# Kernel tuning notes

Measured on AMD Instinct MI355X. Metric: run time of the kernel, lower is better.

## Reference

```python
import jax, jax.numpy as jnp
import numpy as np

B, H, W, EMB = 8, 128, 128, 6
NF = 256  # number_of_filters


def setup_inputs() -> dict:
    key = jax.random.key(0)
    ks = jax.random.split(key, 12)
    s = 0.02  # init_func-style small normal init
    image = jax.random.normal(ks[0], (B, 1, H, W), jnp.float32)
    mask_embedding = jax.random.normal(ks[1], (B, EMB, H, W), jnp.float32)
    # conv stack: 134->256 (s2), 256->512 (s2), 512->1024 (s2), 1024->1024 (s2), avgpool8, 1024->128 (1x1)
    w0 = jax.random.normal(ks[2], (NF, W + EMB, 4, 4), jnp.float32) * s
    b0 = jnp.zeros((NF,), jnp.float32)
    w1 = jax.random.normal(ks[3], (2 * NF, NF, 4, 4), jnp.float32) * s
    b1 = jnp.zeros((2 * NF,), jnp.float32)
    w2 = jax.random.normal(ks[4], (4 * NF, 2 * NF, 4, 4), jnp.float32) * s
    b2 = jnp.zeros((4 * NF,), jnp.float32)
    w3 = jax.random.normal(ks[5], (4 * NF, 4 * NF, 4, 4), jnp.float32) * s
    b3 = jnp.zeros((4 * NF,), jnp.float32)
    w4 = jax.random.normal(ks[6], (W, 4 * NF, 1, 1), jnp.float32) * s
    b4 = jnp.zeros((W,), jnp.float32)
    return dict(image=image, mask_embedding=mask_embedding,
                w0=w0, b0=b0, w1=w1, b1=b1, w2=w2, b2=b2, w3=w3, b3=b3, w4=w4, b4=b4)


def _spectral_map(image, mask_embedding):
    # Original: kspace = fft2(image); for each column i zero out all other k-space
    # columns, ifft2 (unnormalized torch.ifft => 1/(H*W)), take real part.
    # Since only column i is nonzero, ifft2 separates:
    #   sep[b,i,h,w] = Re( (1/W) * ifft_H(kspace[:, :, i])[h] * exp(2j*pi*w*i/W) )
    Bv, _, Hv, Wv = image.shape
    kspace = jnp.fft.fft2(image[:, 0])                    # (B, H, W) complex64
    col = jnp.fft.ifft(kspace, axis=1) / Wv               # (B, H, W_i); ifft over height gives 1/H
    idx = jnp.arange(Wv)
    twiddle = jnp.exp((2j * jnp.pi / Wv) * jnp.outer(idx, idx).astype(jnp.float32))  # (W_spatial, W_i) complex64
    sep = jnp.real(jnp.einsum('bhi,wi->bihw', col, twiddle))  # (B, W, H, W) float32
    return jnp.concatenate([sep, mask_embedding], axis=1)     # (B, W+EMB, H, W)


def _conv(x, w, b, stride):
    y = jax.lax.conv_general_dilated(x, w, (stride, stride), [(1, 1), (1, 1)],
                                     dimension_numbers=('NCHW', 'OIHW', 'NCHW'))
    return y + b[None, :, None, None]


def _inorm(x):  # InstanceNorm2d, affine=False, eps=1e-5
    m = jnp.mean(x, (2, 3), keepdims=True)
    v = jnp.var(x, (2, 3), keepdims=True)
    return (x - m) * jax.lax.rsqrt(v + 1e-5)


def _lrelu(x):
    return jax.nn.leaky_relu(x, 0.2)


def reference(image, mask_embedding, w0, b0, w1, b1, w2, b2, w3, b3, w4, b4):
    x = _spectral_map(image, mask_embedding)       # (B, 134, 128, 128)
    x = _lrelu(_conv(x, w0, b0, 2))                # (B, 256, 64, 64)
    x = _lrelu(_inorm(_conv(x, w1, b1, 2)))        # (B, 512, 32, 32)
    x = _lrelu(_inorm(_conv(x, w2, b2, 2)))        # (B, 1024, 16, 16)
    x = _lrelu(_inorm(_conv(x, w3, b3, 2)))        # (B, 1024, 8, 8)
    pooled = jnp.mean(x, (2, 3))                   # AvgPool(k=8) -> (B, 1024)
    out = jnp.einsum('bc,oc->bo', pooled, w4[:, :, 0, 0]) + b4  # 1x1 conv + squeeze -> (B, 128)
    return out
```

## Files before the change

kernel.cpp:

```cpp
#include <hip/hip_runtime.h>
#include <hip/hip_bf16.h>
#include <cstdint>
#include <cstddef>

typedef __attribute__((ext_vector_type(8))) short bf16x8;
typedef __attribute__((ext_vector_type(4))) float f32x4;

#define PI2F 6.283185307179586f

__device__ __forceinline__ float bf2f(unsigned short u) {
  union { float f; uint32_t i; } x; x.i = ((uint32_t)u) << 16; return x.f;
}
__device__ __forceinline__ unsigned short f2bf(float f) {
  union { float f; uint32_t i; } x; x.f = f;
  uint32_t r = x.i + 0x7FFF + ((x.i >> 16) & 1);
  return (unsigned short)(r >> 16);
}

__device__ __forceinline__ void glds16(const void* g, void* l) {
  __builtin_amdgcn_global_load_lds(
      (const __attribute__((address_space(1))) unsigned int*)g,
      (__attribute__((address_space(3))) unsigned int*)l, 16, 0, 0);
}

__global__ void zinit_kernel(unsigned short* __restrict__ zp, unsigned short* __restrict__ pad) {
  int t = threadIdx.x;
  zp[t] = 0;
  pad[t] = 0;
}

__global__ void dft_kernel(const float* __restrict__ img, float2* __restrict__ col,
                           float2* __restrict__ tw) {
  __shared__ float row[128];
  __shared__ float2 twl[128];
  const int bh = blockIdx.x;
  const int i = threadIdx.x;
  row[i] = img[bh * 128 + i];
  float s, c;
  sincosf(PI2F * (float)i / 128.0f, &s, &c);
  twl[i] = make_float2(c, s);
  __syncthreads();
  if (bh == 0) tw[i] = twl[i];
  float sr = 0.f, si = 0.f;
  for (int w = 0; w < 128; ++w) {
    float v = row[w];
    float2 t = twl[(i * w) & 127];
    sr += v * t.x;
    si -= v * t.y;
  }
  col[bh * 128 + i] = make_float2(sr * (1.0f / 128.0f), si * (1.0f / 128.0f));
}

__global__ __launch_bounds__(256)
void sep_cl2_kernel(const float2* __restrict__ col, const float2* __restrict__ tw,
                    const float* __restrict__ maskE, unsigned short* __restrict__ x0) {
  __shared__ float2 cl[128];
  __shared__ float2 twl[128];
  const int bh = blockIdx.x;
  const int b = bh >> 7, h = bh & 127;
  const int tid = threadIdx.x;
  if (tid < 128) {
    cl[tid] = col[(b * 128 + h) * 128 + tid];
    twl[tid] = tw[tid];
  }
  __syncthreads();
  const int p = tid >> 1;
  const int c0 = (tid & 1) * 64;
  unsigned short* dst = x0 + ((size_t)bh * 128 + p) * 144;
#pragma unroll
  for (int j = 0; j < 16; ++j) {
    ushort4 o;
#pragma unroll
    for (int q = 0; q < 4; ++q) {
      int c = c0 + 4 * j + q;
      float2 cv = cl[c];
      float2 t = twl[(p * c) & 127];
      float v = cv.x * t.x - cv.y * t.y;
      ((unsigned short*)&o)[q] = f2bf(v);
    }
    *reinterpret_cast<ushort4*>(dst + c0 + 4 * j) = o;
  }
  if (tid < 128) {
    const int w = tid;
    float v[6];
#pragma unroll
    for (int cm = 0; cm < 6; ++cm)
      v[cm] = maskE[(((size_t)(b * 6 + cm) * 128) + h) * 128 + w];
    unsigned short* d2 = x0 + ((size_t)bh * 128 + w) * 144 + 128;
    ushort4 m0, m1, mz;
    m0.x = f2bf(v[0]); m0.y = f2bf(v[1]); m0.z = f2bf(v[2]); m0.w = f2bf(v[3]);
    m1.x = f2bf(v[4]); m1.y = f2bf(v[5]); m1.z = 0; m1.w = 0;
    mz.x = 0; mz.y = 0; mz.z = 0; mz.w = 0;
    reinterpret_cast<ushort4*>(d2)[0] = m0;
    reinterpret_cast<ushort4*>(d2)[1] = m1;
    reinterpret_cast<ushort4*>(d2)[2] = mz;
    reinterpret_cast<ushort4*>(d2)[3] = mz;
  }
}

template<int CIN, int CINP>
__global__ __launch_bounds__(256)
void cvtperm_kernel(const float* __restrict__ src, unsigned short* __restrict__ dst) {
  __shared__ unsigned short tile[16][68];
  const int m = blockIdx.y;
  const int ci0 = blockIdx.x * 64;
  const int tid = threadIdx.x;
  {
    const int ci = ci0 + (tid >> 2);
    const int t0 = (tid & 3) * 4;
    float4 v = make_float4(0.f, 0.f, 0.f, 0.f);
    if (ci < CIN) v = *reinterpret_cast<const float4*>(&src[((size_t)m * CIN + ci) * 16 + t0]);
    const int cr = tid >> 2;
    tile[t0 + 0][cr] = f2bf(v.x);
    tile[t0 + 1][cr] = f2bf(v.y);
    tile[t0 + 2][cr] = f2bf(v.z);
    tile[t0 + 3][cr] = f2bf(v.w);
  }
  __syncthreads();
  {
    const int t = tid >> 4;
    const int co = (tid & 15) * 4;
    const int ci = ci0 + co;
    if (ci < CINP) {
      ushort4 o;
      o.x = tile[t][co]; o.y = tile[t][co + 1]; o.z = tile[t][co + 2]; o.w = tile[t][co + 3];
      *reinterpret_cast<ushort4*>(&dst[(size_t)m * (16 * CINP) + (size_t)t * CINP + ci]) = o;
    }
  }
}

template<int CINP, int CSTOR, int COUT, int HI, int WI, int HO, int WO, int NSPLIT, bool FUSED>
__global__ __launch_bounds__(128, 2)
void conv_cl6_kernel(const unsigned short* __restrict__ X,
                     const unsigned short* __restrict__ Wt,
                     const unsigned short* __restrict__ zp,
                     const float* __restrict__ bias,
                     unsigned short* __restrict__ Y,
                     float* __restrict__ P) {
  constexpr int KTOT = 16 * CINP;
  constexpr int CPT = CINP / 32;
  constexpr int HOWO = HO * WO;
  constexpr int LHW = __builtin_ctz(HOWO);
  constexpr int LWO = __builtin_ctz(WO);
  constexpr int TPS = 16 / NSPLIT;
  constexpr size_t PSTRIDE = (size_t)8 * HOWO * COUT;
  constexpr int NIT = TPS * CPT;

  __shared__ __align__(16) unsigned short As[3][4096];
  __shared__ __align__(16) unsigned short Bs[3][2048];

  const int tid = threadIdx.x;
  const int lane = tid & 63;
  const int wv = tid >> 6;
  const int n0 = blockIdx.x * 64;
  const int m0 = blockIdx.y * 128;
  const int split = blockIdx.z;
  const int r = lane & 15, g = lane >> 4;
  const int slot = (((g + ((r >> 1) & 3)) & 3)) * 8;

  const int sr = tid >> 2;
  const int chk = tid & 3;
  const int kofs = (((chk - ((sr >> 1) & 3)) & 3)) * 8;

  int bb0, bho0, bwo0, bb1, bho1, bwo1;
  {
    int rn0 = n0 + sr, rn1 = n0 + sr + 32;
    bb0 = rn0 >> LHW; bb1 = rn1 >> LHW;
    int re0 = rn0 & (HOWO - 1), re1 = rn1 & (HOWO - 1);
    bho0 = re0 >> LWO; bho1 = re1 >> LWO;
    bwo0 = re0 & (WO - 1); bwo1 = re1 & (WO - 1);
  }

  const int tap0 = split * TPS;
  int tapI = tap0, ccI = 0;
  size_t boff0, boff1; bool bok0, bok1;
  auto tap_geom = [&](int t) {
    int kh = t >> 2, kw = t & 3;
    {
      int h = 2 * bho0 - 1 + kh, w = 2 * bwo0 - 1 + kw;
      bool hv = (unsigned)h < (unsigned)HI, wvv = (unsigned)w < (unsigned)WI;
      bok0 = hv && wvv;
      boff0 = (((size_t)bb0 * HI + (hv ? h : 0)) * WI + (wvv ? w : 0)) * (size_t)CSTOR;
    }
    {
      int h = 2 * bho1 - 1 + kh, w = 2 * bwo1 - 1 + kw;
      bool hv = (unsigned)h < (unsigned)HI, wvv = (unsigned)w < (unsigned)WI;
      bok1 = hv && wvv;
      boff1 = (((size_t)bb1 * HI + (hv ? h : 0)) * WI + (wvv ? w : 0)) * (size_t)CSTOR;
    }
  };
  tap_geom(tapI);

  auto issue = [&](int buf) {
    const int kk = tapI * CINP + ccI * 32 + kofs;
    const unsigned short* wb = Wt + (size_t)(m0 + sr) * KTOT + kk;
    glds16(wb,                       &As[buf][(wv * 16) * 32]);
    glds16(wb + (size_t)32 * KTOT,   &As[buf][(32 + wv * 16) * 32]);
    glds16(wb + (size_t)64 * KTOT,   &As[buf][(64 + wv * 16) * 32]);
    glds16(wb + (size_t)96 * KTOT,   &As[buf][(96 + wv * 16) * 32]);
    const int ci = ccI * 32 + kofs;
    glds16(bok0 ? (X + boff0 + ci) : zp, &Bs[buf][(wv * 16) * 32]);
    glds16(bok1 ? (X + boff1 + ci) : zp, &Bs[buf][(32 + wv * 16) * 32]);
  };
  auto advance = [&]() {
    ccI++;
    if (ccI == CPT) { ccI = 0; tapI++; if (tapI < tap0 + TPS) tap_geom(tapI); }
  };

  f32x4 acc[4][4] = {};

  issue(0); advance();
  issue(1); advance();

  int buf = 0, nbuf = 2;
  for (int it = 0; it < NIT; ++it) {
    if (it + 1 < NIT) asm volatile("s_waitcnt vmcnt(6)" ::: "memory");
    else              asm volatile("s_waitcnt vmcnt(0)" ::: "memory");
    __builtin_amdgcn_s_barrier();
    __builtin_amdgcn_sched_barrier(0);
    if (it + 2 < NIT) { issue(nbuf); advance(); }
    bf16x8 af[4], bf[4];
#pragma unroll
    for (int mi = 0; mi < 4; ++mi)
      af[mi] = *reinterpret_cast<const bf16x8*>(&As[buf][(wv * 64 + mi * 16 + r) * 32 + slot]);
#pragma unroll
    for (int ni = 0; ni < 4; ++ni)
      bf[ni] = *reinterpret_cast<const bf16x8*>(&Bs[buf][(ni * 16 + r) * 32 + slot]);
    __builtin_amdgcn_s_setprio(1);
#pragma unroll
    for (int mi = 0; mi < 4; ++mi)
#pragma unroll
      for (int ni = 0; ni < 4; ++ni)
        acc[mi][ni] = __builtin_amdgcn_mfma_f32_16x16x32_bf16(af[mi], bf[ni], acc[mi][ni], 0, 0, 0);
    __builtin_amdgcn_s_setprio(0);
    buf = buf == 2 ? 0 : buf + 1;
    nbuf = nbuf == 2 ? 0 : nbuf + 1;
  }

#pragma unroll
  for (int ni = 0; ni < 4; ++ni) {
    int n = n0 + ni * 16 + r;
    int b = n >> LHW;
    int rem = n & (HOWO - 1);
    size_t obase = ((size_t)b * HOWO + rem) * COUT;
#pragma unroll
    for (int mi = 0; mi < 4; ++mi) {
      int mb = m0 + wv * 64 + mi * 16 + g * 4;
      f32x4 a = acc[mi][ni];
      if constexpr (FUSED) {
        float v0 = a[0] + bias[mb + 0]; v0 = v0 > 0.f ? v0 : 0.2f * v0;
        float v1 = a[1] + bias[mb + 1]; v1 = v1 > 0.f ? v1 : 0.2f * v1;
        float v2 = a[2] + bias[mb + 2]; v2 = v2 > 0.f ? v2 : 0.2f * v2;
        float v3 = a[3] + bias[mb + 3]; v3 = v3 > 0.f ? v3 : 0.2f * v3;
        ushort4 o;
        o.x = f2bf(v0); o.y = f2bf(v1); o.z = f2bf(v2); o.w = f2bf(v3);
        *reinterpret_cast<ushort4*>(&Y[obase + mb]) = o;
      } else {
        *reinterpret_cast<float4*>(&P[split * PSTRIDE + obase + mb]) =
            make_float4(a[0], a[1], a[2], a[3]);
      }
    }
  }
}

template<int HOWO, int COUT, int NSPLIT>
__global__ __launch_bounds__(256)
void inorm_cl3_kernel(const float* __restrict__ P, unsigned short* __restrict__ Y) {
  constexpr int PER = HOWO / 32;
  constexpr size_t PSTRIDE = (size_t)8 * HOWO * COUT;
  const int b = blockIdx.y;
  const int cl = threadIdx.x & 7;
  const int c = blockIdx.x * 8 + cl;
  const int hw0 = threadIdx.x >> 3;
  const float* base = P + ((size_t)b * HOWO) * COUT + c;
  float v[PER];
  float s1 = 0.f, s2 = 0.f;
#pragma unroll
  for (int j = 0; j < PER; ++j) {
    int hw = hw0 + j * 32;
    float x = 0.f;
#pragma unroll
    for (int s = 0; s < NSPLIT; ++s) x += base[s * PSTRIDE + (size_t)hw * COUT];
    v[j] = x; s1 += x; s2 += x * x;
  }
  __shared__ float r1[32][9], r2[32][9];
  __shared__ float ms[8], rs[8];
  r1[hw0][cl] = s1; r2[hw0][cl] = s2;
  __syncthreads();
  if (threadIdx.x < 8) {
    float a1 = 0.f, a2 = 0.f;
#pragma unroll
    for (int i = 0; i < 32; ++i) { a1 += r1[i][threadIdx.x]; a2 += r2[i][threadIdx.x]; }
    float mean = a1 * (1.0f / HOWO);
    float var = a2 * (1.0f / HOWO) - mean * mean;
    ms[threadIdx.x] = mean;
    rs[threadIdx.x] = rsqrtf(var + 1e-5f);
  }
  __syncthreads();
  const float mean = ms[cl], rstd = rs[cl];
  unsigned short* yb = Y + ((size_t)b * HOWO) * COUT + c;
#pragma unroll
  for (int j = 0; j < PER; ++j) {
    int hw = hw0 + j * 32;
    float t = (v[j] - mean) * rstd;
    t = t > 0.f ? t : 0.2f * t;
    yb[(size_t)hw * COUT] = f2bf(t);
  }
}

__global__ __launch_bounds__(256)
void pool_cl_kernel(const unsigned short* __restrict__ X, float* __restrict__ pooled) {
  const int b = blockIdx.x;
  const int c4 = threadIdx.x * 4;
  float4 acc = make_float4(0.f, 0.f, 0.f, 0.f);
  for (int hw = 0; hw < 64; ++hw) {
    ushort4 v = *reinterpret_cast<const ushort4*>(&X[((size_t)b * 64 + hw) * 1024 + c4]);
    acc.x += bf2f(v.x); acc.y += bf2f(v.y); acc.z += bf2f(v.z); acc.w += bf2f(v.w);
  }
  acc.x *= (1.0f / 64.0f); acc.y *= (1.0f / 64.0f);
  acc.z *= (1.0f / 64.0f); acc.w *= (1.0f / 64.0f);
  *reinterpret_cast<float4*>(&pooled[b * 1024 + c4]) = acc;
}

__global__ __launch_bounds__(64)
void fc_kernel(const float* __restrict__ pooled, const float* __restrict__ w4,
               const float* __restrict__ b4, float* __restrict__ out) {
  const int bo = blockIdx.x;
  const int b = bo >> 7, o = bo & 127;
  const int lane = threadIdx.x;
  float s = 0.f;
#pragma unroll
  for (int j = 0; j < 16; ++j) {
    int c = lane + j * 64;
    s += pooled[b * 1024 + c] * w4[o * 1024 + c];
  }
#pragma unroll
  for (int off = 32; off > 0; off >>= 1) s += __shfl_xor(s, off);
  if (lane == 0) out[bo] = s + b4[o];
}

extern "C" void kernel_launch(void* const* d_in, const int* in_sizes, int n_in,
                              void* d_out, int out_size, void* d_ws, size_t ws_size,
                              hipStream_t stream) {
  (void)in_sizes; (void)n_in; (void)out_size; (void)ws_size;
  const float* image = (const float*)d_in[0];
  const float* maskE = (const float*)d_in[1];
  const float* w0 = (const float*)d_in[2];
  const float* b0 = (const float*)d_in[3];
  const float* w1 = (const float*)d_in[4];
  const float* w2 = (const float*)d_in[6];
  const float* w3 = (const float*)d_in[8];
  const float* w4 = (const float*)d_in[10];
  const float* b4 = (const float*)d_in[11];
  float* out = (float*)d_out;

  char* ws = (char*)d_ws;
  size_t off = 0;
  auto alloc = [&](size_t bytes) -> void* {
    void* p = ws + off;
    off = (off + bytes + 255) & ~(size_t)255;
    return p;
  };

  const size_t X0BYTES = (size_t)8 * 128 * 128 * 144 * 2;
  unsigned short* wbuf = (unsigned short*)alloc((size_t)1024 * 16384 * 2);
  char* bufA = (char*)alloc(X0BYTES + 256);
  char* bufB = (char*)alloc((size_t)8 * 4096 * 256 * 2);
  float2* col = (float2*)alloc((size_t)131072 * sizeof(float2));
  float2* tw = (float2*)alloc(128 * sizeof(float2));
  float* pooled = (float*)alloc(8192 * 4);
  unsigned short* zp = (unsigned short*)alloc(256);

  unsigned short* x0 = (unsigned short*)bufA;
  unsigned short* x0pad = (unsigned short*)(bufA + X0BYTES);
  float* part = (float*)bufA;
  unsigned short* a0 = (unsigned short*)bufB;
  unsigned short* a1 = (unsigned short*)bufB;
  unsigned short* a2 = (unsigned short*)bufB;
  unsigned short* a3 = (unsigned short*)bufB;

  zinit_kernel<<<1, 128, 0, stream>>>(zp, x0pad);

  dft_kernel<<<1024, 128, 0, stream>>>(image, col, tw);
  sep_cl2_kernel<<<1024, 256, 0, stream>>>(col, tw, maskE, x0);

  cvtperm_kernel<134, 160><<<dim3(3, 256), 256, 0, stream>>>(w0, wbuf);
  conv_cl6_kernel<160, 144, 256, 128, 128, 64, 64, 1, true>
      <<<dim3(512, 2, 1), 128, 0, stream>>>(x0, wbuf, zp, b0, a0, nullptr);

  cvtperm_kernel<256, 256><<<dim3(4, 512), 256, 0, stream>>>(w1, wbuf);
  conv_cl6_kernel<256, 256, 512, 64, 64, 32, 32, 2, false>
      <<<dim3(128, 4, 2), 128, 0, stream>>>(a0, wbuf, zp, nullptr, nullptr, part);
  inorm_cl3_kernel<1024, 512, 2><<<dim3(64, 8), 256, 0, stream>>>(part, a1);

  cvtperm_kernel<512, 512><<<dim3(8, 1024), 256, 0, stream>>>(w2, wbuf);
  conv_cl6_kernel<512, 512, 1024, 32, 32, 16, 16, 4, false>
      <<<dim3(32, 8, 4), 128, 0, stream>>>(a1, wbuf, zp, nullptr, nullptr, part);
  inorm_cl3_kernel<256, 1024, 4><<<dim3(128, 8), 256, 0, stream>>>(part, a2);

  cvtperm_kernel<1024, 1024><<<dim3(16, 1024), 256, 0, stream>>>(w3, wbuf);
  conv_cl6_kernel<1024, 1024, 1024, 16, 16, 8, 8, 16, false>
      <<<dim3(8, 8, 16), 128, 0, stream>>>(a2, wbuf, zp, nullptr, nullptr, part);
  inorm_cl3_kernel<64, 1024, 16><<<dim3(128, 8), 256, 0, stream>>>(part, a3);

  pool_cl_kernel<<<8, 256, 0, stream>>>(a3, pooled);
  fc_kernel<<<1024, 64, 0, stream>>>(pooled, w4, b4, out);
}
```

Measured before the change: 368.7 us.

## Use 4 waves per conv block with 2x2 warp tiling and double buffering

The implicit-GEMM conv kernel moves from 2 waves (each computing 64x64) to 4 waves arranged 2x2 (each computing 64x32). Each thread now issues fewer async global-to-LDS loads, and the accumulator count per thread is halved. The pipeline drops from triple buffering with explicit vmcnt waits to double buffering with a plain __syncthreads, which shrinks LDS use and allows higher occupancy. The cost is less prefetch depth, so global load latency is hidden less well, and the setprio hints are removed.

```diff
diff --git a/kernel.cpp b/kernel.cpp
--- a/kernel.cpp
+++ b/kernel.cpp
@@ -130,8 +130,8 @@
 }
 
 template<int CINP, int CSTOR, int COUT, int HI, int WI, int HO, int WO, int NSPLIT, bool FUSED>
-__global__ __launch_bounds__(128, 2)
-void conv_cl6_kernel(const unsigned short* __restrict__ X,
+__global__ __launch_bounds__(256, 4)
+void conv_cl7_kernel(const unsigned short* __restrict__ X,
                      const unsigned short* __restrict__ Wt,
                      const unsigned short* __restrict__ zp,
                      const float* __restrict__ bias,
@@ -146,12 +146,13 @@
   constexpr size_t PSTRIDE = (size_t)8 * HOWO * COUT;
   constexpr int NIT = TPS * CPT;
 
-  __shared__ __align__(16) unsigned short As[3][4096];
-  __shared__ __align__(16) unsigned short Bs[3][2048];
+  __shared__ __align__(16) unsigned short As[2][4096];
+  __shared__ __align__(16) unsigned short Bs[2][2048];
 
   const int tid = threadIdx.x;
   const int lane = tid & 63;
   const int wv = tid >> 6;
+  const int wm = wv >> 1, wn = wv & 1;
   const int n0 = blockIdx.x * 64;
   const int m0 = blockIdx.y * 128;
   const int split = blockIdx.z;
@@ -162,90 +163,70 @@
   const int chk = tid & 3;
   const int kofs = (((chk - ((sr >> 1) & 3)) & 3)) * 8;
 
-  int bb0, bho0, bwo0, bb1, bho1, bwo1;
+  int bb, bho, bwo;
   {
-    int rn0 = n0 + sr, rn1 = n0 + sr + 32;
-    bb0 = rn0 >> LHW; bb1 = rn1 >> LHW;
-    int re0 = rn0 & (HOWO - 1), re1 = rn1 & (HOWO - 1);
-    bho0 = re0 >> LWO; bho1 = re1 >> LWO;
-    bwo0 = re0 & (WO - 1); bwo1 = re1 & (WO - 1);
+    int rn = n0 + sr;
+    bb = rn >> LHW;
+    int re = rn & (HOWO - 1);
+    bho = re >> LWO;
+    bwo = re & (WO - 1);
   }
 
   const int tap0 = split * TPS;
   int tapI = tap0, ccI = 0;
-  size_t boff0, boff1; bool bok0, bok1;
+  size_t boff; bool bok;
   auto tap_geom = [&](int t) {
     int kh = t >> 2, kw = t & 3;
-    {
-      int h = 2 * bho0 - 1 + kh, w = 2 * bwo0 - 1 + kw;
-      bool hv = (unsigned)h < (unsigned)HI, wvv = (unsigned)w < (unsigned)WI;
-      bok0 = hv && wvv;
-      boff0 = (((size_t)bb0 * HI + (hv ? h : 0)) * WI + (wvv ? w : 0)) * (size_t)CSTOR;
-    }
-    {
-      int h = 2 * bho1 - 1 + kh, w = 2 * bwo1 - 1 + kw;
-      bool hv = (unsigned)h < (unsigned)HI, wvv = (unsigned)w < (unsigned)WI;
-      bok1 = hv && wvv;
-      boff1 = (((size_t)bb1 * HI + (hv ? h : 0)) * WI + (wvv ? w : 0)) * (size_t)CSTOR;
-    }
+    int h = 2 * bho - 1 + kh, w = 2 * bwo - 1 + kw;
+    bool hv = (unsigned)h < (unsigned)HI, wvv = (unsigned)w < (unsigned)WI;
+    bok = hv && wvv;
+    boff = (((size_t)bb * HI + (hv ? h : 0)) * WI + (wvv ? w : 0)) * (size_t)CSTOR;
   };
   tap_geom(tapI);
 
   auto issue = [&](int buf) {
     const int kk = tapI * CINP + ccI * 32 + kofs;
     const unsigned short* wb = Wt + (size_t)(m0 + sr) * KTOT + kk;
-    glds16(wb,                       &As[buf][(wv * 16) * 32]);
-    glds16(wb + (size_t)32 * KTOT,   &As[buf][(32 + wv * 16) * 32]);
-    glds16(wb + (size_t)64 * KTOT,   &As[buf][(64 + wv * 16) * 32]);
-    glds16(wb + (size_t)96 * KTOT,   &As[buf][(96 + wv * 16) * 32]);
+    glds16(wb,                     &As[buf][wv * 512]);
+    glds16(wb + (size_t)64 * KTOT, &As[buf][2048 + wv * 512]);
     const int ci = ccI * 32 + kofs;
-    glds16(bok0 ? (X + boff0 + ci) : zp, &Bs[buf][(wv * 16) * 32]);
-    glds16(bok1 ? (X + boff1 + ci) : zp, &Bs[buf][(32 + wv * 16) * 32]);
+    glds16(bok ? (X + boff + ci) : zp, &Bs[buf][wv * 512]);
   };
   auto advance = [&]() {
     ccI++;
     if (ccI == CPT) { ccI = 0; tapI++; if (tapI < tap0 + TPS) tap_geom(tapI); }
   };
 
-  f32x4 acc[4][4] = {};
+  f32x4 acc[4][2] = {};
 
   issue(0); advance();
-  issue(1); advance();
-
-  int buf = 0, nbuf = 2;
   for (int it = 0; it < NIT; ++it) {
-    if (it + 1 < NIT) asm volatile("s_waitcnt vmcnt(6)" ::: "memory");
-    else              asm volatile("s_waitcnt vmcnt(0)" ::: "memory");
-    __builtin_amdgcn_s_barrier();
-    __builtin_amdgcn_sched_barrier(0);
-    if (it + 2 < NIT) { issue(nbuf); advance(); }
-    bf16x8 af[4], bf[4];
+    __syncthreads();
+    if (it + 1 < NIT) { issue((it + 1) & 1); advance(); }
+    const int buf = it & 1;
+    bf16x8 af[4], bf[2];
 #pragma unroll
     for (int mi = 0; mi < 4; ++mi)
-      af[mi] = *reinterpret_cast<const bf16x8*>(&As[buf][(wv * 64 + mi * 16 + r) * 32 + slot]);
-#pragma unroll
-    for (int ni = 0; ni < 4; ++ni)
-      bf[ni] = *reinterpret_cast<const bf16x8*>(&Bs[buf][(ni * 16 + r) * 32 + slot]);
-    __builtin_amdgcn_s_setprio(1);
+      af[mi] = *reinterpret_cast<const bf16x8*>(&As[buf][(wm * 64 + mi * 16 + r) * 32 + slot]);
+#pragma unroll
+    for (int ni = 0; ni < 2; ++ni)
+      bf[ni] = *reinterpret_cast<const bf16x8*>(&Bs[buf][(wn * 32 + ni * 16 + r) * 32 + slot]);
 #pragma unroll
     for (int mi = 0; mi < 4; ++mi)
 #pragma unroll
-      for (int ni = 0; ni < 4; ++ni)
+      for (int ni = 0; ni < 2; ++ni)
         acc[mi][ni] = __builtin_amdgcn_mfma_f32_16x16x32_bf16(af[mi], bf[ni], acc[mi][ni], 0, 0, 0);
-    __builtin_amdgcn_s_setprio(0);
-    buf = buf == 2 ? 0 : buf + 1;
-    nbuf = nbuf == 2 ? 0 : nbuf + 1;
-  }
-
-#pragma unroll
-  for (int ni = 0; ni < 4; ++ni) {
-    int n = n0 + ni * 16 + r;
+  }
+
+#pragma unroll
+  for (int ni = 0; ni < 2; ++ni) {
+    int n = n0 + wn * 32 + ni * 16 + r;
     int b = n >> LHW;
     int rem = n & (HOWO - 1);
     size_t obase = ((size_t)b * HOWO + rem) * COUT;
 #pragma unroll
     for (int mi = 0; mi < 4; ++mi) {
-      int mb = m0 + wv * 64 + mi * 16 + g * 4;
+      int mb = m0 + wm * 64 + mi * 16 + g * 4;
       f32x4 a = acc[mi][ni];
       if constexpr (FUSED) {
         float v0 = a[0] + bias[mb + 0]; v0 = v0 > 0.f ? v0 : 0.2f * v0;
@@ -385,22 +366,22 @@
   sep_cl2_kernel<<<1024, 256, 0, stream>>>(col, tw, maskE, x0);
 
   cvtperm_kernel<134, 160><<<dim3(3, 256), 256, 0, stream>>>(w0, wbuf);
-  conv_cl6_kernel<160, 144, 256, 128, 128, 64, 64, 1, true>
-      <<<dim3(512, 2, 1), 128, 0, stream>>>(x0, wbuf, zp, b0, a0, nullptr);
+  conv_cl7_kernel<160, 144, 256, 128, 128, 64, 64, 1, true>
+      <<<dim3(512, 2, 1), 256, 0, stream>>>(x0, wbuf, zp, b0, a0, nullptr);
 
   cvtperm_kernel<256, 256><<<dim3(4, 512), 256, 0, stream>>>(w1, wbuf);
-  conv_cl6_kernel<256, 256, 512, 64, 64, 32, 32, 2, false>
-      <<<dim3(128, 4, 2), 128, 0, stream>>>(a0, wbuf, zp, nullptr, nullptr, part);
+  conv_cl7_kernel<256, 256, 512, 64, 64, 32, 32, 2, false>
+      <<<dim3(128, 4, 2), 256, 0, stream>>>(a0, wbuf, zp, nullptr, nullptr, part);
   inorm_cl3_kernel<1024, 512, 2><<<dim3(64, 8), 256, 0, stream>>>(part, a1);
 
   cvtperm_kernel<512, 512><<<dim3(8, 1024), 256, 0, stream>>>(w2, wbuf);
-  conv_cl6_kernel<512, 512, 1024, 32, 32, 16, 16, 4, false>
-      <<<dim3(32, 8, 4), 128, 0, stream>>>(a1, wbuf, zp, nullptr, nullptr, part);
+  conv_cl7_kernel<512, 512, 1024, 32, 32, 16, 16, 4, false>
+      <<<dim3(32, 8, 4), 256, 0, stream>>>(a1, wbuf, zp, nullptr, nullptr, part);
   inorm_cl3_kernel<256, 1024, 4><<<dim3(128, 8), 256, 0, stream>>>(part, a2);
 
   cvtperm_kernel<1024, 1024><<<dim3(16, 1024), 256, 0, stream>>>(w3, wbuf);
-  conv_cl6_kernel<1024, 1024, 1024, 16, 16, 8, 8, 16, false>
-      <<<dim3(8, 8, 16), 128, 0, stream>>>(a2, wbuf, zp, nullptr, nullptr, part);
+  conv_cl7_kernel<1024, 1024, 1024, 16, 16, 8, 8, 16, false>
+      <<<dim3(8, 8, 16), 256, 0, stream>>>(a2, wbuf, zp, nullptr, nullptr, part);
   inorm_cl3_kernel<64, 1024, 16><<<dim3(128, 8), 256, 0, stream>>>(part, a3);
 
   pool_cl_kernel<<<8, 256, 0, stream>>>(a3, pooled);
```

After: 367.8 us. No clear change (-0.2%).
